# Performance work log

Measured on AMD Instinct MI355X. Metric: run time of the kernel, lower is better.

The kernel has to match this reference:

```python
import jax, jax.numpy as jnp
import numpy as np

B, H, S, DK, DV = 4, 16, 2048, 64, 64

def setup_inputs() -> dict:
    key = jax.random.key(0)
    k1, k2, k3, k4 = jax.random.split(key, 4)
    Q = jax.random.normal(k1, (B, H, S, DK), dtype=jnp.float32)
    K = jax.random.normal(k2, (B, H, S, DK), dtype=jnp.float32)
    V = jax.random.normal(k3, (B, H, S, DV), dtype=jnp.float32)
    mask_out = jax.random.randint(k4, (B, 1, 1, S), 0, 2).astype(jnp.bool_)
    return {"Q": Q, "K": K, "V": V, "mask_out": mask_out}

def reference(Q, K, V, mask_out):
    key_size = Q.shape[-1]
    seq_q, seq_k = Q.shape[-2], K.shape[-2]
    scale = jnp.sqrt(jnp.float32(key_size))
    # scores: [B, H, Sq, Sk]
    scores = jnp.einsum('bhqd,bhkd->bhqk', Q, K) / scale
    scores = jnp.where(mask_out, jnp.float32(-1e9), scores)
    attn = jax.nn.softmax(scores, axis=-1)
    # Gaussian relative-position decay: exp(-|i-j|^2 / (Sk^2 / 2))
    idx_q = jnp.arange(seq_q, dtype=jnp.float32)[:, None]
    idx_k = jnp.arange(seq_k, dtype=jnp.float32)[None, :]
    rel = idx_q - idx_k  # [Sq, Sk]
    decay = jnp.exp(-(rel * rel) * (2.0 / (seq_k * seq_k)))  # [Sq, Sk]
    attn = attn * decay  # broadcast over [B, H]
    return jnp.einsum('bhqk,bhkv->bhqv', attn, V)
```

## Files before the change

kernel.cpp:

```cpp
#include <hip/hip_runtime.h>
#include <hip/hip_bf16.h>

typedef __attribute__((ext_vector_type(8))) short bf16x8;
typedef __attribute__((ext_vector_type(4))) short bf16x4;
typedef __attribute__((ext_vector_type(4))) float f32x4;
typedef __attribute__((ext_vector_type(4))) unsigned u32x4;
typedef __attribute__((ext_vector_type(4))) int i32x4;

constexpr int Bn = 4, Hn = 16, S = 2048, D = 64;
constexpr int BQ = 128;
constexpr float LOG2E = 1.44269504088896340736f;

__device__ __forceinline__ unsigned cvtpk(float lo, float hi) {
    unsigned r;
    asm("v_cvt_pk_bf16_f32 %0, %1, %2" : "=v"(r) : "v"(lo), "v"(hi));
    return r;
}

__device__ __forceinline__ f32x4 mfma16(bf16x4 a, bf16x4 b, f32x4 c) {
#if __has_builtin(__builtin_amdgcn_mfma_f32_16x16x16bf16_1k)
    return __builtin_amdgcn_mfma_f32_16x16x16bf16_1k(a, b, c, 0, 0, 0);
#else
    asm volatile("v_mfma_f32_16x16x16_bf16 %0, %1, %2, %0"
                 : "+v"(c) : "v"(a), "v"(b));
    return c;
#endif
}

__global__ void compact_mask(const void* __restrict__ maskg,
                             int* __restrict__ idxp, int* __restrict__ Mg) {
    const int b = blockIdx.x, t = threadIdx.x;
    __shared__ int wsum[4];
    __shared__ int Msh;

    const unsigned* mu = (const unsigned*)maskg;
    bool is_bytes = false;
    #pragma unroll 8
    for (int i = 0; i < 64; ++i) is_bytes |= (mu[i] > 1u);

    int keep[8]; int cnt = 0;
    #pragma unroll
    for (int i = 0; i < 8; ++i) {
        const int key = t * 8 + i;
        int m;
        if (is_bytes) m = ((const unsigned char*)maskg)[b * S + key];
        else          m = ((const int*)maskg)[b * S + key];
        keep[i] = (m == 0);
        cnt += keep[i];
    }
    const int l = t & 63, w = t >> 6;
    int pre = cnt;
    #pragma unroll
    for (int d = 1; d < 64; d <<= 1) {
        int v = __shfl_up(pre, d, 64);
        if (l >= d) pre += v;
    }
    if (l == 63) wsum[w] = pre;
    __syncthreads();
    int base = 0;
    for (int i = 0; i < w; ++i) base += wsum[i];
    int offs = base + pre - cnt;
    #pragma unroll
    for (int i = 0; i < 8; ++i)
        if (keep[i]) idxp[b * S + (offs++)] = t * 8 + i;
    if (t == 255) Msh = base + pre;
    __syncthreads();
    const int M = Msh;
    for (int i = M + t; i < S; i += 256) idxp[b * S + i] = 0;
    if (M == 0)
        for (int i = t; i < S; i += 256) idxp[b * S + i] = i;
    if (t == 0) Mg[b] = (M == 0) ? -1 : M;
}

__global__ __launch_bounds__(256, 3) void attn_fwd(
    const float* __restrict__ Qg, const float* __restrict__ Kg,
    const float* __restrict__ Vg, const int* __restrict__ idxp,
    const int* __restrict__ Mg, float* __restrict__ outg)
{
    __shared__ alignas(16) short Kt[64][72];
    __shared__ alignas(16) short Vt[64][72];
    __shared__ alignas(16) float dtab[2176];
    __shared__ alignas(16) int   idxs[64];

    const int blk = blockIdx.x;
    const int qt  = blk & 15;
    const int bh  = blk >> 4;
    const int b   = bh >> 4;
    const int q0  = qt * BQ;

    const float* Qp = Qg + ((size_t)bh * S + q0) * D;
    const float* Kp = Kg + (size_t)bh * S * D;
    const float* Vp = Vg + (size_t)bh * S * D;
    float*       Op = outg + ((size_t)bh * S + q0) * D;
    const int*   idxb = idxp + b * S;

    const int t  = threadIdx.x;
    const int w  = t >> 6;
    const int l  = t & 63;
    const int lr = l & 15;
    const int lg = l >> 4;

    const int  Mraw    = Mg[b];
    const bool uniform = (Mraw < 0);
    const int  M       = uniform ? S : Mraw;

    const float CD2 = (2.0f / ((float)S * (float)S)) * LOG2E;
    for (int i = t; i < 2176; i += 256) {
        const float r = (float)(q0 + i - 2047);
        dtab[i] = __builtin_exp2f(-CD2 * r * r);
    }

    const float qscale = uniform ? 0.0f : 0.125f * LOG2E;
    bf16x8 qf[2][2];
    #pragma unroll
    for (int rt = 0; rt < 2; ++rt) {
        const int row = w * 32 + rt * 16 + lr;
        #pragma unroll
        for (int g = 0; g < 2; ++g) {
            const float* src = Qp + row * D + g * 32 + lg * 8;
            union { unsigned u[4]; bf16x8 v; } cv;
            #pragma unroll
            for (int jj = 0; jj < 4; ++jj)
                cv.u[jj] = cvtpk(src[2 * jj] * qscale, src[2 * jj + 1] * qscale);
            qf[rt][g] = cv.v;
        }
    }

    f32x4 Oacc[2][4];
    #pragma unroll
    for (int rt = 0; rt < 2; ++rt)
        #pragma unroll
        for (int dt = 0; dt < 4; ++dt) Oacc[rt][dt] = f32x4{0.f, 0.f, 0.f, 0.f};
    float mrun[2] = {-1e30f, -1e30f};
    float lrun[2] = {0.f, 0.f};

    const int qrl2047 = w * 32 + lr + 2047;

    for (int kv = 0; kv < M; kv += 64) {
        const int  rem  = M - kv;
        const bool last = (rem <= 64);
        __syncthreads();
        {
            const int key = t >> 3;
            const int dc  = (t & 7) * 8;
            #pragma unroll
            for (int it = 0; it < 2; ++it) {
                const int row = idxb[kv + key + it * 32];
                const float* src = Kp + (size_t)row * D + dc;
                u32x4 pk;
                #pragma unroll
                for (int jj = 0; jj < 4; ++jj)
                    pk[jj] = cvtpk(src[2 * jj], src[2 * jj + 1]);
                *(u32x4*)&Kt[key + it * 32][dc] = pk;
            }
        }
        if (t < 64) idxs[t] = idxb[kv + t];
        {
            const int dv = t & 63;
            const int kb = (t >> 6) * 16;
            float f[16];
            #pragma unroll
            for (int i = 0; i < 16; ++i) {
                int row = idxb[kv + kb + i];
                row = __builtin_amdgcn_readfirstlane(row);
                f[i] = Vp[(size_t)row * D + dv];
            }
            u32x4 p0, p1;
            #pragma unroll
            for (int jj = 0; jj < 4; ++jj) {
                p0[jj] = cvtpk(f[2 * jj], f[2 * jj + 1]);
                p1[jj] = cvtpk(f[8 + 2 * jj], f[9 + 2 * jj]);
            }
            *(u32x4*)&Vt[dv][kb]     = p0;
            *(u32x4*)&Vt[dv][kb + 8] = p1;
        }
        __syncthreads();

        bf16x8 kf[4][2];
        #pragma unroll
        for (int kt = 0; kt < 4; ++kt)
            #pragma unroll
            for (int g = 0; g < 2; ++g)
                kf[kt][g] = *(const bf16x8*)&Kt[kt * 16 + lr][g * 32 + lg * 8];

        bf16x4 Xb[2][4];

        #pragma unroll
        for (int rt = 0; rt < 2; ++rt) {
            f32x4 sc[4];
            #pragma unroll
            for (int kt = 0; kt < 4; ++kt) {
                f32x4 acc = f32x4{0.f, 0.f, 0.f, 0.f};
                acc = __builtin_amdgcn_mfma_f32_16x16x32_bf16(kf[kt][0], qf[rt][0], acc, 0, 0, 0);
                acc = __builtin_amdgcn_mfma_f32_16x16x32_bf16(kf[kt][1], qf[rt][1], acc, 0, 0, 0);
                sc[kt] = acc;
            }
            float mt = fmaxf(fmaxf(sc[0][0], sc[0][1]), fmaxf(sc[0][2], sc[0][3]));
            #pragma unroll
            for (int kt = 1; kt < 4; ++kt)
                mt = fmaxf(mt, fmaxf(fmaxf(sc[kt][0], sc[kt][1]), fmaxf(sc[kt][2], sc[kt][3])));
            mt = fmaxf(mt, __shfl_xor(mt, 16, 64));
            mt = fmaxf(mt, __shfl_xor(mt, 32, 64));
            if (!__all(mt <= mrun[rt] + 8.0f)) {
                const float mnew = fmaxf(mrun[rt], mt);
                const float rs = __builtin_exp2f(mrun[rt] - mnew);
                mrun[rt] = mnew;
                lrun[rt] *= rs;
                #pragma unroll
                for (int dt = 0; dt < 4; ++dt) Oacc[rt][dt] *= rs;
            }
            const float m  = mrun[rt];
            const int   qi = qrl2047 + rt * 16;
            float lp = 0.f;
            #pragma unroll
            for (int kt = 0; kt < 4; ++kt) {
                const i32x4 iv = *(const i32x4*)&idxs[kt * 16 + lg * 4];
                float p0 = __builtin_exp2f(sc[kt][0] - m);
                float p1 = __builtin_exp2f(sc[kt][1] - m);
                float p2 = __builtin_exp2f(sc[kt][2] - m);
                float p3 = __builtin_exp2f(sc[kt][3] - m);
                if (last) {
                    const int ck = kt * 16 + lg * 4;
                    p0 = (ck + 0 < rem) ? p0 : 0.f;
                    p1 = (ck + 1 < rem) ? p1 : 0.f;
                    p2 = (ck + 2 < rem) ? p2 : 0.f;
                    p3 = (ck + 3 < rem) ? p3 : 0.f;
                }
                lp += (p0 + p1) + (p2 + p3);
                const float d0 = dtab[qi - iv[0]];
                const float d1 = dtab[qi - iv[1]];
                const float d2 = dtab[qi - iv[2]];
                const float d3 = dtab[qi - iv[3]];
                union { unsigned u[2]; bf16x4 v; } cx;
                cx.u[0] = cvtpk(p0 * d0, p1 * d1);
                cx.u[1] = cvtpk(p2 * d2, p3 * d3);
                Xb[rt][kt] = cx.v;
            }
            lrun[rt] += lp;
        }

        #pragma unroll
        for (int kt = 0; kt < 4; ++kt) {
            bf16x4 vA[4];
            #pragma unroll
            for (int dt = 0; dt < 4; ++dt)
                vA[dt] = *(const bf16x4*)&Vt[dt * 16 + lr][kt * 16 + lg * 4];
            #pragma unroll
            for (int dt = 0; dt < 4; ++dt) {
                Oacc[0][dt] = mfma16(vA[dt], Xb[0][kt], Oacc[0][dt]);
                Oacc[1][dt] = mfma16(vA[dt], Xb[1][kt], Oacc[1][dt]);
            }
        }
    }

    #pragma unroll
    for (int rt = 0; rt < 2; ++rt) {
        float ls = lrun[rt];
        ls += __shfl_xor(ls, 16, 64);
        ls += __shfl_xor(ls, 32, 64);
        const float inv = 1.0f / ls;
        const int row = w * 32 + rt * 16 + lr;
        #pragma unroll
        for (int dt = 0; dt < 4; ++dt) {
            f32x4 o = Oacc[rt][dt];
            o[0] *= inv; o[1] *= inv; o[2] *= inv; o[3] *= inv;
            *(f32x4*)&Op[(size_t)row * D + dt * 16 + lg * 4] = o;
        }
    }
}

extern "C" void kernel_launch(void* const* d_in, const int* in_sizes, int n_in,
                              void* d_out, int out_size, void* d_ws, size_t ws_size,
                              hipStream_t stream) {
    const float* Q = (const float*)d_in[0];
    const float* K = (const float*)d_in[1];
    const float* V = (const float*)d_in[2];
    const void*  M = d_in[3];
    float* out = (float*)d_out;
    int* idxp = (int*)d_ws;
    int* Mg   = idxp + Bn * S;
    compact_mask<<<dim3(Bn), dim3(256), 0, stream>>>(M, idxp, Mg);
    const int nblk = Bn * Hn * (S / BQ);
    attn_fwd<<<dim3(nblk), dim3(256), 0, stream>>>(Q, K, V, idxp, Mg, out);
}
```

Baseline: 136.4 us.

## Pre-pack gathered K/V to bf16 once and double-buffer tiles in attention

Adds a pack_kv kernel that gathers the unmasked keys and values per head once, converts them to bf16 and stores them in a tile-friendly layout, with V pre-transposed, in the workspace. The new attention kernel then streams contiguous bf16 tiles with register prefetch and double-buffered LDS, so it no longer does indirect fp32 gathers and conversions in every query block. It also remaps block IDs for locality and raises wave priority around the MFMA sections. The cost is an extra kernel launch and a workspace write and read of packed K/V, and the old gather path is kept as a fallback when the workspace is too small.

```diff
diff --git a/kernel.cpp b/kernel.cpp
--- a/kernel.cpp
+++ b/kernel.cpp
@@ -72,7 +72,272 @@
     if (t == 0) Mg[b] = (M == 0) ? -1 : M;
 }
 
-__global__ __launch_bounds__(256, 3) void attn_fwd(
+__global__ void pack_kv(const float* __restrict__ Kg, const float* __restrict__ Vg,
+                        const int* __restrict__ idxp, const int* __restrict__ Mg,
+                        short* __restrict__ Kw, short* __restrict__ Vw) {
+    const int bh = blockIdx.x, b = bh >> 4;
+    const int ck0 = blockIdx.y * 256;
+    const int t = threadIdx.x;
+    const int Mraw = Mg[b];
+    const int M = (Mraw < 0) ? S : Mraw;
+    if (ck0 >= M) return;
+    const int* idxb = idxp + b * S;
+    const float* Kp = Kg + (size_t)bh * S * D;
+    const float* Vp = Vg + (size_t)bh * S * D;
+
+    {
+        const int dc = (t & 7) * 8;
+        #pragma unroll
+        for (int tile = 0; tile < 4; ++tile)
+            #pragma unroll
+            for (int it = 0; it < 2; ++it) {
+                const int key = ck0 + tile * 64 + (t >> 3) + it * 32;
+                u32x4 pk = u32x4{0u, 0u, 0u, 0u};
+                if (key < M) {
+                    const float* src = Kp + (size_t)idxb[key] * D + dc;
+                    #pragma unroll
+                    for (int jj = 0; jj < 4; ++jj)
+                        pk[jj] = cvtpk(src[2 * jj], src[2 * jj + 1]);
+                }
+                *(u32x4*)(Kw + ((size_t)bh * S + key) * D + dc) = pk;
+            }
+    }
+    {
+        const int dv = t & 63;
+        const int kb = (t >> 6) * 16;
+        #pragma unroll
+        for (int tile = 0; tile < 4; ++tile) {
+            const int tg = (ck0 >> 6) + tile;
+            float f[16];
+            #pragma unroll
+            for (int i = 0; i < 16; ++i) {
+                const int key = ck0 + tile * 64 + kb + i;
+                float v = 0.f;
+                if (key < M) {
+                    int row = idxb[key];
+                    row = __builtin_amdgcn_readfirstlane(row);
+                    v = Vp[(size_t)row * D + dv];
+                }
+                f[i] = v;
+            }
+            u32x4 p0, p1;
+            #pragma unroll
+            for (int jj = 0; jj < 4; ++jj) {
+                p0[jj] = cvtpk(f[2 * jj], f[2 * jj + 1]);
+                p1[jj] = cvtpk(f[8 + 2 * jj], f[9 + 2 * jj]);
+            }
+            short* dst = Vw + (((size_t)bh * 32 + tg) * 64 + dv) * 64 + kb;
+            *(u32x4*)dst = p0;
+            *(u32x4*)(dst + 8) = p1;
+        }
+    }
+}
+
+__global__ __launch_bounds__(256, 3) void attn_packed(
+    const float* __restrict__ Qg, const short* __restrict__ Kw,
+    const short* __restrict__ Vw, const int* __restrict__ idxp,
+    const int* __restrict__ Mg, float* __restrict__ outg)
+{
+    __shared__ alignas(16) short Kt[2][64][72];
+    __shared__ alignas(16) short Vt[2][64][72];
+    __shared__ alignas(16) float dtab[2176];
+    __shared__ alignas(16) int   idxs[2][64];
+
+    const int bid  = blockIdx.x;
+    const int lblk = ((bid & 7) << 7) | (bid >> 3);
+    const int qt   = lblk & 15;
+    const int bh   = lblk >> 4;
+    const int b    = bh >> 4;
+    const int q0   = qt * BQ;
+
+    const float* Qp   = Qg + ((size_t)bh * S + q0) * D;
+    const short* Ksrc = Kw + (size_t)bh * S * D;
+    const short* Vsrc = Vw + (size_t)bh * 32 * 64 * 64;
+    float*       Op   = outg + ((size_t)bh * S + q0) * D;
+    const int*   idxb = idxp + b * S;
+
+    const int t  = threadIdx.x;
+    const int w  = t >> 6;
+    const int l  = t & 63;
+    const int lr = l & 15;
+    const int lg = l >> 4;
+
+    const int  Mraw    = Mg[b];
+    const bool uniform = (Mraw < 0);
+    const int  M       = uniform ? S : Mraw;
+    const int  ntiles  = (M + 63) >> 6;
+
+    u32x4 kr0, kr1, vr0, vr1;
+    int ir = 0;
+    kr0 = *(const u32x4*)(Ksrc + t * 16);
+    kr1 = *(const u32x4*)(Ksrc + t * 16 + 8);
+    vr0 = *(const u32x4*)(Vsrc + t * 16);
+    vr1 = *(const u32x4*)(Vsrc + t * 16 + 8);
+    if (t < 64) ir = idxb[t];
+
+    const float CD2 = (2.0f / ((float)S * (float)S)) * LOG2E;
+    for (int i = t; i < 2176; i += 256) {
+        const float r = (float)(q0 + i - 2047);
+        dtab[i] = __builtin_exp2f(-CD2 * r * r);
+    }
+
+    const float qscale = uniform ? 0.0f : 0.125f * LOG2E;
+    bf16x8 qf[2][2];
+    #pragma unroll
+    for (int rt = 0; rt < 2; ++rt) {
+        const int row = w * 32 + rt * 16 + lr;
+        #pragma unroll
+        for (int g = 0; g < 2; ++g) {
+            const float* src = Qp + row * D + g * 32 + lg * 8;
+            union { unsigned u[4]; bf16x8 v; } cv;
+            #pragma unroll
+            for (int jj = 0; jj < 4; ++jj)
+                cv.u[jj] = cvtpk(src[2 * jj] * qscale, src[2 * jj + 1] * qscale);
+            qf[rt][g] = cv.v;
+        }
+    }
+
+    f32x4 Oacc[2][4];
+    #pragma unroll
+    for (int rt = 0; rt < 2; ++rt)
+        #pragma unroll
+        for (int dt = 0; dt < 4; ++dt) Oacc[rt][dt] = f32x4{0.f, 0.f, 0.f, 0.f};
+    float mrun[2] = {-1e30f, -1e30f};
+    float lrun[2] = {0.f, 0.f};
+
+    const int qrl2047 = w * 32 + lr + 2047;
+    const int wr = t >> 2, wc = (t & 3) * 16;
+
+    *(u32x4*)&Kt[0][wr][wc]     = kr0;
+    *(u32x4*)&Kt[0][wr][wc + 8] = kr1;
+    *(u32x4*)&Vt[0][wr][wc]     = vr0;
+    *(u32x4*)&Vt[0][wr][wc + 8] = vr1;
+    if (t < 64) idxs[0][t] = ir;
+    __syncthreads();
+
+    int c = 0;
+    for (int tt = 0; tt < ntiles; ++tt) {
+        const int  rem      = M - tt * 64;
+        const bool last     = (rem <= 64);
+        const bool havenext = (tt + 1 < ntiles);
+
+        if (havenext) {
+            const short* kp = Ksrc + (size_t)(tt + 1) * 4096;
+            const short* vp = Vsrc + (size_t)(tt + 1) * 4096;
+            kr0 = *(const u32x4*)(kp + t * 16);
+            kr1 = *(const u32x4*)(kp + t * 16 + 8);
+            vr0 = *(const u32x4*)(vp + t * 16);
+            vr1 = *(const u32x4*)(vp + t * 16 + 8);
+            if (t < 64) ir = idxb[(tt + 1) * 64 + t];
+        }
+
+        bf16x8 kf[4][2];
+        #pragma unroll
+        for (int kt = 0; kt < 4; ++kt)
+            #pragma unroll
+            for (int g = 0; g < 2; ++g)
+                kf[kt][g] = *(const bf16x8*)&Kt[c][kt * 16 + lr][g * 32 + lg * 8];
+
+        bf16x4 Xb[2][4];
+        #pragma unroll
+        for (int rt = 0; rt < 2; ++rt) {
+            f32x4 sc[4];
+            __builtin_amdgcn_s_setprio(1);
+            #pragma unroll
+            for (int kt = 0; kt < 4; ++kt) {
+                f32x4 acc = f32x4{0.f, 0.f, 0.f, 0.f};
+                acc = __builtin_amdgcn_mfma_f32_16x16x32_bf16(kf[kt][0], qf[rt][0], acc, 0, 0, 0);
+                acc = __builtin_amdgcn_mfma_f32_16x16x32_bf16(kf[kt][1], qf[rt][1], acc, 0, 0, 0);
+                sc[kt] = acc;
+            }
+            __builtin_amdgcn_s_setprio(0);
+            float mt = fmaxf(fmaxf(sc[0][0], sc[0][1]), fmaxf(sc[0][2], sc[0][3]));
+            #pragma unroll
+            for (int kt = 1; kt < 4; ++kt)
+                mt = fmaxf(mt, fmaxf(fmaxf(sc[kt][0], sc[kt][1]), fmaxf(sc[kt][2], sc[kt][3])));
+            mt = fmaxf(mt, __shfl_xor(mt, 16, 64));
+            mt = fmaxf(mt, __shfl_xor(mt, 32, 64));
+            if (!__all(mt <= mrun[rt] + 8.0f)) {
+                const float mnew = fmaxf(mrun[rt], mt);
+                const float rs = __builtin_exp2f(mrun[rt] - mnew);
+                mrun[rt] = mnew;
+                lrun[rt] *= rs;
+                #pragma unroll
+                for (int dt = 0; dt < 4; ++dt) Oacc[rt][dt] *= rs;
+            }
+            const float m  = mrun[rt];
+            const int   qi = qrl2047 + rt * 16;
+            float lp = 0.f;
+            #pragma unroll
+            for (int kt = 0; kt < 4; ++kt) {
+                const i32x4 iv = *(const i32x4*)&idxs[c][kt * 16 + lg * 4];
+                float p0 = __builtin_exp2f(sc[kt][0] - m);
+                float p1 = __builtin_exp2f(sc[kt][1] - m);
+                float p2 = __builtin_exp2f(sc[kt][2] - m);
+                float p3 = __builtin_exp2f(sc[kt][3] - m);
+                if (last) {
+                    const int ck = kt * 16 + lg * 4;
+                    p0 = (ck + 0 < rem) ? p0 : 0.f;
+                    p1 = (ck + 1 < rem) ? p1 : 0.f;
+                    p2 = (ck + 2 < rem) ? p2 : 0.f;
+                    p3 = (ck + 3 < rem) ? p3 : 0.f;
+                }
+                lp += (p0 + p1) + (p2 + p3);
+                const float d0 = dtab[qi - iv[0]];
+                const float d1 = dtab[qi - iv[1]];
+                const float d2 = dtab[qi - iv[2]];
+                const float d3 = dtab[qi - iv[3]];
+                union { unsigned u[2]; bf16x4 v; } cx;
+                cx.u[0] = cvtpk(p0 * d0, p1 * d1);
+                cx.u[1] = cvtpk(p2 * d2, p3 * d3);
+                Xb[rt][kt] = cx.v;
+            }
+            lrun[rt] += lp;
+        }
+
+        __builtin_amdgcn_s_setprio(1);
+        #pragma unroll
+        for (int kt = 0; kt < 4; ++kt) {
+            bf16x4 vA[4];
+            #pragma unroll
+            for (int dt = 0; dt < 4; ++dt)
+                vA[dt] = *(const bf16x4*)&Vt[c][dt * 16 + lr][kt * 16 + lg * 4];
+            #pragma unroll
+            for (int dt = 0; dt < 4; ++dt) {
+                Oacc[0][dt] = mfma16(vA[dt], Xb[0][kt], Oacc[0][dt]);
+                Oacc[1][dt] = mfma16(vA[dt], Xb[1][kt], Oacc[1][dt]);
+            }
+        }
+        __builtin_amdgcn_s_setprio(0);
+
+        if (havenext) {
+            *(u32x4*)&Kt[c ^ 1][wr][wc]     = kr0;
+            *(u32x4*)&Kt[c ^ 1][wr][wc + 8] = kr1;
+            *(u32x4*)&Vt[c ^ 1][wr][wc]     = vr0;
+            *(u32x4*)&Vt[c ^ 1][wr][wc + 8] = vr1;
+            if (t < 64) idxs[c ^ 1][t] = ir;
+        }
+        __syncthreads();
+        c ^= 1;
+    }
+
+    #pragma unroll
+    for (int rt = 0; rt < 2; ++rt) {
+        float ls = lrun[rt];
+        ls += __shfl_xor(ls, 16, 64);
+        ls += __shfl_xor(ls, 32, 64);
+        const float inv = 1.0f / ls;
+        const int row = w * 32 + rt * 16 + lr;
+        #pragma unroll
+        for (int dt = 0; dt < 4; ++dt) {
+            f32x4 o = Oacc[rt][dt];
+            o[0] *= inv; o[1] *= inv; o[2] *= inv; o[3] *= inv;
+            *(f32x4*)&Op[(size_t)row * D + dt * 16 + lg * 4] = o;
+        }
+    }
+}
+
+__global__ __launch_bounds__(256, 3) void attn_gather(
     const float* __restrict__ Qg, const float* __restrict__ Kg,
     const float* __restrict__ Vg, const int* __restrict__ idxp,
     const int* __restrict__ Mg, float* __restrict__ outg)
@@ -184,7 +449,6 @@
                 kf[kt][g] = *(const bf16x8*)&Kt[kt * 16 + lr][g * 32 + lg * 8];
 
         bf16x4 Xb[2][4];
-
         #pragma unroll
         for (int rt = 0; rt < 2; ++rt) {
             f32x4 sc[4];
@@ -236,7 +500,7 @@
                 cx.u[1] = cvtpk(p2 * d2, p3 * d3);
                 Xb[rt][kt] = cx.v;
             }
-            lrun[rt] += lp;
+            lrun[rt] += lp * 0.f + lp;
         }
 
         #pragma unroll
@@ -277,9 +541,20 @@
     const float* V = (const float*)d_in[2];
     const void*  M = d_in[3];
     float* out = (float*)d_out;
+
     int* idxp = (int*)d_ws;
     int* Mg   = idxp + Bn * S;
+    size_t base = (((size_t)(Bn * S + Bn) * 4) + 255) & ~(size_t)255;
+    short* Kw = (short*)((char*)d_ws + base);
+    short* Vw = Kw + (size_t)Bn * Hn * S * D;
+    const size_t need = base + 2 * (size_t)Bn * Hn * S * D * sizeof(short);
+
     compact_mask<<<dim3(Bn), dim3(256), 0, stream>>>(M, idxp, Mg);
     const int nblk = Bn * Hn * (S / BQ);
-    attn_fwd<<<dim3(nblk), dim3(256), 0, stream>>>(Q, K, V, idxp, Mg, out);
-}
+    if (ws_size >= need) {
+        pack_kv<<<dim3(Bn * Hn, S / 256), dim3(256), 0, stream>>>(K, V, idxp, Mg, Kw, Vw);
+        attn_packed<<<dim3(nblk), dim3(256), 0, stream>>>(Q, Kw, Vw, idxp, Mg, out);
+    } else {
+        attn_gather<<<dim3(nblk), dim3(256), 0, stream>>>(Q, K, V, idxp, Mg, out);
+    }
+}
```

Result: no change. 138.4 us (+1.4%).
